# Optimization experiments

Measured on AMD Instinct MI355X. Metric: run time of the kernel, lower is better.

Reference implementation:

```python
import jax, jax.numpy as jnp
from jax import lax
import numpy as np

B, T, N = 32, 64, 128
D = 64            # d_model = d_in
C = 2 * D + 1     # combined dim = 129
CK = C // 8       # per-head q/k dim = 16
H = 2             # num_heads
QD = 5            # query_vector_dim
NE = 8            # node_emb_dim
PLM = 768         # plm_rep_dim
ALPHA = 0.5       # rarity_alpha
NEG = -9e15       # masked_fill value from source


def setup_inputs() -> dict:
    key = jax.random.key(0)
    ks = jax.random.split(key, 20)

    def u(i, shape, fan):
        s = float(np.sqrt(1.0 / fan))
        return jax.random.uniform(ks[i], shape, jnp.float32, -s, s)

    return dict(
        obs_emb=jax.random.normal(ks[0], (B, T, N, D), jnp.float32),
        observed_mask=(jax.random.uniform(ks[1], (B, T, N)) < 0.3).astype(jnp.float32),
        avg_interval=jax.random.uniform(ks[2], (B, T, N), jnp.float32, 0.0, 10.0),
        var_plm_rep_tensor=jax.random.normal(ks[3], (N, PLM), jnp.float32),
        lengths=jax.random.randint(ks[4], (B, 1), T // 2, T + 1).astype(jnp.int32),
        rarity_W=jax.random.normal(ks[5], (N, N), jnp.float32),
        pf_W1=u(6, (PLM, 2 * D), PLM), pf_b1=jnp.zeros((2 * D,), jnp.float32),
        pf_W2=u(7, (2 * D, QD), 2 * D), pf_b2=jnp.zeros((QD,), jnp.float32),
        pg_W1=u(8, (PLM, 2 * D), PLM), pg_b1=jnp.zeros((2 * D,), jnp.float32),
        pg_W2=u(9, (2 * D, NE), 2 * D), pg_b2=jnp.zeros((NE,), jnp.float32),
        rst_W=u(10, (QD, C, D), C), rst_b=u(11, (QD, D), QD),
        upd_W=u(12, (QD, C, D), C), upd_b=u(13, (QD, D), QD),
        cand_W=u(14, (QD, C, D), C), cand_b=u(15, (QD, D), QD),
        q_W=u(16, (H, C, CK), C), q_b=jnp.zeros((H, CK), jnp.float32),
        k_W=u(17, (H, C, CK), C), k_b=jnp.zeros((H, CK), jnp.float32),
        v_W=u(18, (H, C, C), C), v_b=jnp.zeros((H, C), jnp.float32),
    )


def reference(obs_emb, observed_mask, avg_interval, var_plm_rep_tensor,
              rarity_W, pf_W1, pf_b1, pf_W2, pf_b2, pg_W1, pg_b1, pg_W2, pg_b2,
              rst_W, rst_b, upd_W, upd_b, cand_W, cand_b,
              q_W, q_b, k_W, k_b, v_W, v_b, lengths):
    # variable query vectors & node embeddings (identical for every batch element)
    qv = jax.nn.relu(var_plm_rep_tensor @ pf_W1 + pf_b1) @ pf_W2 + pf_b2   # [N,QD]
    ne = jax.nn.relu(var_plm_rep_tensor @ pg_W1 + pg_b1) @ pg_W2 + pg_b2   # [N,NE]
    ne = ne / jnp.maximum(jnp.linalg.norm(ne, axis=-1, keepdims=True), 1e-12)
    adj = jax.nn.softmax(ne @ ne.T, axis=-1)                               # [N,N] static base adjacency
    var_total_obs = observed_mask.sum(axis=1)                               # [B,N]
    I = jnp.eye(N, dtype=obs_emb.dtype)
    inv_sqrt = 1.0 / np.sqrt(CK)

    def gate(z, W, b):
        # hypernetwork-generated per-node affine (MLP_Param): z [B,N,C] -> [B,N,D]
        return jnp.einsum('bnc,qco,nq->bno', z, W, qv) + qv @ b

    def step(carry, xs):
        h, out = carry
        cur_obs, cur_mask, cur_avg, t = xs
        rar = ALPHA * jnp.tanh(cur_avg / (var_total_obs + 1.0))             # [B,N]
        rmat = -rarity_W[None] * jnp.abs(rar[:, :, None] - rar[:, None, :])  # [B,N,N]
        amask = cur_mask[:, :, None] * cur_mask[:, None, :]                  # obs outer-product mask
        cur_adj = adj[None] * (1.0 + rmat) * amask * (1.0 - I) + I
        x = jnp.concatenate([cur_obs, rar[..., None]], axis=-1)             # [B,N,D+1]
        comb = jnp.concatenate([x, h], axis=-1)                              # [B,N,C]
        q = jnp.einsum('bnc,hck->bhnk', comb, q_W) + q_b[None, :, None, :]
        k = jnp.einsum('bnc,hck->bhnk', comb, k_W) + k_b[None, :, None, :]
        v = jnp.einsum('bnc,hcd->bhnd', comb, v_W) + v_b[None, :, None, :]
        s = jnp.einsum('bhnk,bhmk->bhnm', q, k) * inv_sqrt
        s = jax.nn.leaky_relu(s, 0.2)
        s = jnp.where(cur_adj[:, None, :, :] == 0, NEG, s)                   # use_adj_mask=True
        att = jnp.einsum('bhnm,bhmd->bhnd', jax.nn.softmax(s, axis=-1), v).mean(axis=1)  # [B,N,C]
        obs = (cur_mask > 0)[..., None]
        r = jax.nn.sigmoid(gate(att, rst_W, rst_b))
        u = jax.nn.sigmoid(gate(att, upd_W, upd_b))
        h1 = jnp.where(obs, r * h, h)                                        # h[nodes_ind] = r*h[nodes_ind]
        cand = jnp.tanh(gate(jnp.concatenate([x, h1], axis=-1), cand_W, cand_b))
        h2 = jnp.where(obs, (1.0 - u) * h1 + u * cand, h1)                   # scatter update of observed nodes
        fin = (t == lengths[:, 0] - 1)[:, None, None]
        out = jnp.where(fin, h2, out)                                        # capture h at end of each sample
        return (h2, out), None

    h0 = jnp.zeros((B, N, D), obs_emb.dtype)
    xs = (jnp.swapaxes(obs_emb, 0, 1), jnp.swapaxes(observed_mask, 0, 1),
          jnp.swapaxes(avg_interval, 0, 1), jnp.arange(T))
    (_, out), _ = lax.scan(step, (h0, h0), xs)
    return out
```

## Files before the change

### kernel.cpp

```cpp
#include <hip/hip_runtime.h>
#include <math.h>

#define B_   32
#define T_   64
#define N_   128
#define D_   64
#define C_   129
#define CK_  16
#define H_   2
#define QD_  5
#define PLM_ 768

typedef _Float16 h2v __attribute__((ext_vector_type(2)));
typedef _Float16 h4v __attribute__((ext_vector_type(4)));
typedef _Float16 h8  __attribute__((ext_vector_type(8)));
typedef float    f4  __attribute__((ext_vector_type(4)));

constexpr int OFF_QV   = 0;
constexpr int OFF_BE   = 640;
constexpr int OFF_WB2  = OFF_BE + 3*128*64;
constexpr int OFF_VWB2 = OFF_WB2 + 3*128*65*64;
constexpr int OFF_QKB2 = OFF_VWB2 + 2*65*132;
constexpr int OFF_ATTB = OFF_QKB2 + 4*65*16;
constexpr int OFF_VTO  = OFF_ATTB + 132;
constexpr int OFF_H    = OFF_VTO + B_*N_;
constexpr int OFF_CNT  = OFF_H + 2*B_*N_*64;
constexpr int OFF_VWB3 = OFF_CNT + 32;
constexpr int OFF_QKB4 = OFF_VWB3 + 9*9*64*8/2;
constexpr int OFF_QKE  = OFF_QKB4 + 2*2*4*64*8/2;

#if __has_builtin(__builtin_amdgcn_fdot2)
__device__ __forceinline__ float fdot2(h2v a, h2v b, float c) {
    return __builtin_amdgcn_fdot2(a, b, c, false);
}
#else
__device__ __forceinline__ float fdot2(h2v a, h2v b, float c) {
    return c + (float)a.x*(float)b.x + (float)a.y*(float)b.y;
}
#endif


__global__ void k_qv(const float* __restrict__ plm, const float* __restrict__ W1,
                     const float* __restrict__ b1, const float* __restrict__ W2,
                     const float* __restrict__ b2, float* __restrict__ ws) {
    int n = blockIdx.x, j = threadIdx.x;
    __shared__ float hid[128];
    float acc = b1[j];
    for (int p = 0; p < PLM_; ++p) acc += plm[n*PLM_ + p] * W1[p*128 + j];
    hid[j] = fmaxf(acc, 0.f);
    __syncthreads();
    if (j < QD_) {
        float a = b2[j];
        for (int q = 0; q < 128; ++q) a += hid[q] * W2[q*QD_ + j];
        ws[OFF_QV + n*QD_ + j] = a;
    }
}

__global__ void k_weff(const float* __restrict__ rW, const float* __restrict__ uW,
                       const float* __restrict__ cW, const float* __restrict__ rb,
                       const float* __restrict__ ub, const float* __restrict__ cb,
                       float* __restrict__ ws) {
    int g = blockIdx.x >> 7, n = blockIdx.x & 127;
    const float* W  = (g == 0) ? rW : (g == 1) ? uW : cW;
    const float* bb = (g == 0) ? rb : (g == 1) ? ub : cb;
    float qn[QD_];
#pragma unroll
    for (int q = 0; q < QD_; ++q) qn[q] = ws[OFF_QV + n*QD_ + q];
    h2v* WB = (h2v*)(ws + OFF_WB2);
    for (int idx = threadIdx.x; idx < 65*64; idx += 256) {
        int c2 = idx >> 6, o = idx & 63;
        float w0 = 0.f, w1 = 0.f;
#pragma unroll
        for (int q = 0; q < QD_; ++q) w0 += qn[q] * W[(q*C_ + 2*c2)*D_ + o];
        if (2*c2 + 1 < C_) {
#pragma unroll
            for (int q = 0; q < QD_; ++q) w1 += qn[q] * W[(q*C_ + 2*c2 + 1)*D_ + o];
        }
        WB[((g*128 + n)*65 + c2)*64 + o] = h2v{(_Float16)w0, (_Float16)w1};
    }
    if (threadIdx.x < D_) {
        int o = threadIdx.x;
        float acc = 0.f;
#pragma unroll
        for (int q = 0; q < QD_; ++q) acc += qn[q] * bb[q*D_ + o];
        ws[OFF_BE + (g*128 + n)*D_ + o] = acc;
    }
}

__global__ void k_pack(const float* __restrict__ vW, const float* __restrict__ qW,
                       const float* __restrict__ kW, const float* __restrict__ vb,
                       const float* __restrict__ qb, const float* __restrict__ kb,
                       float* __restrict__ ws) {
    int stride = gridDim.x * blockDim.x;
    int t0 = blockIdx.x * blockDim.x + threadIdx.x;
    _Float16* VB = (_Float16*)(ws + OFF_VWB3);
    for (int idx = t0; idx < 9*9*64*8; idx += stride) {
        int j  = idx & 7;
        int l  = (idx >> 3) & 63;
        int rest = idx >> 9;
        int kt = rest % 9, nt = rest / 9;
        int k = kt*32 + (l >> 4)*8 + j;
        int n = nt*16 + (l & 15);
        float v = 0.f;
        if (n < C_) {
            if (k < 264) {
                int h = k / 132, c = k % 132;
                if (c < C_) v = 0.5f * vW[(h*C_ + c)*C_ + n];
            } else if (k == 264) {
                v = 0.5f * (vb[n] + vb[C_ + n]);
            }
        }
        VB[idx] = (_Float16)v;
    }
    _Float16* QK4 = (_Float16*)(ws + OFF_QKB4);
    for (int idx = t0; idx < 2*2*4*64*8; idx += stride) {
        int j = idx & 7, l = (idx >> 3) & 63, kt = (idx >> 9) & 3;
        int h = (idx >> 11) & 1, qk = (idx >> 12) & 1;
        int c = kt*32 + ((l >> 4) & 3)*8 + j, ck = l & 15;
        const float* src = qk ? qW : kW;
        QK4[idx] = (_Float16)src[(h*C_ + c)*CK_ + ck];
    }
    float* QE = ws + OFF_QKE;
    for (int idx = t0; idx < 128; idx += stride) {
        int ck = idx & 15, kind = (idx >> 4) & 1, h = (idx >> 5) & 1, qk = (idx >> 6) & 1;
        const float* src = qk ? qW : kW;
        const float* sb  = qk ? qb : kb;
        QE[idx] = kind ? sb[h*CK_ + ck] : src[(h*C_ + 128)*CK_ + ck];
    }
}

__global__ void k_vto(const float* __restrict__ mask, float* __restrict__ ws) {
    int idx = blockIdx.x * blockDim.x + threadIdx.x;
    if (idx < B_*N_) {
        int b = idx >> 7, n = idx & 127;
        float acc = 0.f;
        for (int t = 0; t < T_; ++t) acc += mask[(b*T_ + t)*N_ + n];
        ws[OFF_VTO + idx] = acc;
    }
}

__global__ void __launch_bounds__(1024, 4) k_main(
    const float* __restrict__ obs, const float* __restrict__ mask,
    const float* __restrict__ avg, const int* __restrict__ lengths,
    const float* __restrict__ qb, const float* __restrict__ kb,
    float* __restrict__ ws, float* __restrict__ out) {
    const int tid = threadIdx.x;
    const int b  = blockIdx.x >> 3;
    const int ng = blockIdx.x & 7;
    const int n0 = ng * 16;

    __shared__ __align__(16) _Float16 comball[128*144];
    __shared__ __align__(16) char regA[8704];
    __shared__ __align__(16) char regB[13824];
    __shared__ float maskL[128];
    __shared__ float h_own[16*64];

    _Float16* sPH    = (_Float16*)regA;
    _Float16* attF   = (_Float16*)regA;
    float*    h1L    = (float*)(regA + 4352);
    _Float16* kall   = (_Float16*)regB;
    _Float16* qf     = (_Float16*)(regB + 12288);
    _Float16* z_lds  = (_Float16*)regB;
    h2v*      candin = (h2v*)regB;

    float* Hx = ws + OFF_H;
    unsigned* CNT = (unsigned*)(ws + OFF_CNT);
    const h2v* WB  = (const h2v*)(ws + OFF_WB2);
    const h8*  VB3 = (const h8*)(ws + OFF_VWB3);
    const h8*  QK4 = (const h8*)(ws + OFF_QKB4);

    for (int i = tid; i < 16*64; i += 1024) h_own[i] = 0.f;
    for (int i = tid; i < 128*15; i += 1024)
        comball[(i/15)*144 + 129 + (i%15)] = (_Float16)0.f;
    const int lenb = lengths[b];
    __syncthreads();

    for (int t = 0; t < T_; ++t) {
        if (t > 0) {
            if (tid == 0) {
                unsigned target = 8u * (unsigned)t;
                while (__hip_atomic_load(&CNT[b], __ATOMIC_RELAXED,
                                         __HIP_MEMORY_SCOPE_AGENT) < target)
                    __builtin_amdgcn_s_sleep(2);
            }
            __syncthreads();
            const float* Hr = Hx + (size_t)((t & 1)*B_ + b)*N_*64;
#pragma unroll
            for (int p = 0; p < 8; ++p) {
                int idx = tid + p*1024;
                int j = idx >> 6, d = idx & 63;
                float hv = ((j >> 4) == ng) ? h_own[(j & 15)*64 + d]
                         : __hip_atomic_load((float*)Hr + idx, __ATOMIC_RELAXED,
                                             __HIP_MEMORY_SCOPE_AGENT);
                comball[j*144 + 65 + d] = (_Float16)hv;
            }
        } else {
#pragma unroll
            for (int p = 0; p < 8; ++p) {
                int idx = tid + p*1024;
                comball[(idx >> 6)*144 + 65 + (idx & 63)] = (_Float16)0.f;
            }
        }
        {
            const float* obsR = obs + (size_t)(b*T_ + t)*N_*D_;
#pragma unroll
            for (int p = 0; p < 8; ++p) {
                int idx = tid + p*1024;
                comball[(idx >> 6)*144 + (idx & 63)] = (_Float16)obsR[idx];
            }
            if (tid < 128) {
                maskL[tid] = mask[(b*T_ + t)*N_ + tid];
                float a = avg[(b*T_ + t)*N_ + tid];
                comball[tid*144 + 64] =
                    (_Float16)(0.5f * tanhf(a / (ws[OFF_VTO + b*N_ + tid] + 1.f)));
            }
        }
        __syncthreads();
        {
            int w = tid >> 6, l = tid & 63, lr = l & 15, lg = l >> 4;
            int nj = (w < 2) ? 2 : 1;
            for (int jb = 0; jb < nj; ++jb) {
                int qk = jb;
                int hh = jb ? w : (w >> 3);
                int rbase = jb ? n0 : (w & 7)*16;
                const h8* Wf = QK4 + ((qk*2 + hh)*4)*64 + l;
                const _Float16* Ab = comball + (rbase + lr)*144;
                f4 acc = {0.f, 0.f, 0.f, 0.f};
#pragma unroll
                for (int kt = 0; kt < 4; ++kt) {
                    h8 a = *(const h8*)(Ab + kt*32 + lg*8);
                    h8 bf = Wf[kt*64];
                    acc = __builtin_amdgcn_mfma_f32_16x16x32_f16(a, bf, acc, 0, 0, 0);
                }
                const float* QE = ws + OFF_QKE + (qk*2 + hh)*32;
                float w128 = QE[lr], wbias = QE[16 + lr];
#pragma unroll
                for (int r = 0; r < 4; ++r) {
                    int row = rbase + lg*4 + r;
                    float v = acc[r] + (float)comball[row*144 + 128] * w128 + wbias;
                    if (jb == 0) kall[(hh*128 + row)*24 + lr] = (_Float16)v;
                    else         qf[(hh*16 + lg*4 + r)*24 + lr] = (_Float16)v;
                }
            }
        }
        __syncthreads();
        {
            int w = tid >> 6, l = tid & 63, lr = l & 15, lg = l >> 4;
            int h = w >> 3, nt = w & 7;
            h8 a = {}, bq = {};
            if (lg < 2) {
                a  = *(const h8*)(qf + (h*16 + lr)*24 + lg*8);
                bq = *(const h8*)(kall + (h*128 + nt*16 + lr)*24 + lg*8);
            }
            f4 s4 = {0.f, 0.f, 0.f, 0.f};
            s4 = __builtin_amdgcn_mfma_f32_16x16x32_f16(a, bq, s4, 0, 0, 0);
            int j = nt*16 + lr;
            float mj = maskL[j];
#pragma unroll
            for (int r = 0; r < 4; ++r) {
                int i = lg*4 + r, ig = n0 + i;
                float v = s4[r] * 0.25f;
                v = v > 0.f ? v : 0.2f*v;
                if (ig != j && (maskL[ig] == 0.f || mj == 0.f)) v = -60000.f;
                sPH[(h*16 + i)*136 + j] = (_Float16)v;
            }
        }
        __syncthreads();
        {
            int wave = tid >> 6, lane = tid & 63;
#pragma unroll
            for (int r = 0; r < 2; ++r) {
                int u = wave*2 + r;
                float x0 = (float)sPH[u*136 + lane], x1 = (float)sPH[u*136 + lane + 64];
                float m = fmaxf(x0, x1);
                for (int off = 32; off > 0; off >>= 1) m = fmaxf(m, __shfl_xor(m, off, 64));
                float e0 = __expf(x0 - m), e1 = __expf(x1 - m);
                float s = e0 + e1;
                for (int off = 32; off > 0; off >>= 1) s += __shfl_xor(s, off, 64);
                float inv = 1.f / s;
                sPH[u*136 + lane] = (_Float16)(e0*inv);
                sPH[u*136 + lane + 64] = (_Float16)(e1*inv);
            }
        }
        __syncthreads();
        {
            if (tid < 384) {
                int i = tid / 24, cc = tid % 24;
                z_lds[i*296 + 264 + cc] = (cc == 0) ? (_Float16)1.0f : (_Float16)0.0f;
            }
            int wv = tid >> 6, l = tid & 63, lr = l & 15, lg = l >> 4;
            for (int tile = wv; tile < 18; tile += 16) {
                int m = tile / 9, n = tile % 9;
                f4 acc = {0.f, 0.f, 0.f, 0.f};
                const _Float16* Arow = sPH + (m*16 + lr)*136 + lg*8;
                const _Float16* Bcol = comball + (lg*8)*144 + n*16 + lr;
#pragma unroll
                for (int kt = 0; kt < 4; ++kt) {
                    h8 a = *(const h8*)(Arow + kt*32);
                    h8 bf;
#pragma unroll
                    for (int j = 0; j < 8; ++j) bf[j] = Bcol[(kt*32 + j)*144];
                    acc = __builtin_amdgcn_mfma_f32_16x16x32_f16(a, bf, acc, 0, 0, 0);
                }
                int cz = n*16 + lr;
                if (cz < 132) {
#pragma unroll
                    for (int r = 0; r < 4; ++r)
                        z_lds[(lg*4 + r)*296 + m*132 + cz] = (_Float16)acc[r];
                }
            }
        }
        __syncthreads();
        {
            int wv = tid >> 6, l = tid & 63, lr = l & 15, lg = l >> 4;
            if (wv < 9) {
                const h8* VB = VB3 + (size_t)wv*9*64 + l;
                f4 acc = {0.f, 0.f, 0.f, 0.f};
                const _Float16* Az = z_lds + lr*296 + lg*8;
#pragma unroll
                for (int kt = 0; kt < 9; ++kt) {
                    h8 a = *(const h8*)(Az + kt*32);
                    h8 bf = VB[kt*64];
                    acc = __builtin_amdgcn_mfma_f32_16x16x32_f16(a, bf, acc, 0, 0, 0);
                }
                int cp = wv*16 + lr;
                if (cp < 132) {
#pragma unroll
                    for (int r = 0; r < 4; ++r)
                        attF[(lg*4 + r)*136 + cp] = (_Float16)acc[r];
                }
            }
        }
        __syncthreads();
        int il = tid >> 6, o = tid & 63, n = n0 + il;
        float uu, h1;
        bool ob;
        {
            const h2v* WR = WB + ((0*128 + n)*65)*64 + o;
            const h2v* WU = WB + ((1*128 + n)*65)*64 + o;
            float aR = ws[OFF_BE + (0*128 + n)*64 + o];
            float aU = ws[OFF_BE + (1*128 + n)*64 + o];
            const h2v* ar = (const h2v*)(attF + il*136);
#pragma unroll 5
            for (int c2 = 0; c2 < 65; ++c2) {
                h2v a2 = ar[c2];
                aR = fdot2(a2, WR[(size_t)c2*64], aR);
                aU = fdot2(a2, WU[(size_t)c2*64], aU);
            }
            float rg = 1.f/(1.f + __expf(-aR));
            uu = 1.f/(1.f + __expf(-aU));
            ob = maskL[n] > 0.f;
            float h0 = h_own[il*64 + o];
            h1 = ob ? rg*h0 : h0;
            h1L[il*66 + o] = h1;
        }
        __syncthreads();
        {
#pragma unroll
            for (int p = 0; p < 2; ++p) {
                int idx = tid + p*1024;
                if (idx < 1040) {
                    int il2 = idx / 65, cw = idx % 65;
                    int c0 = 2*cw, c1 = 2*cw + 1;
                    int j = n0 + il2;
                    float v0 = (c0 < 65) ? (float)comball[j*144 + c0]
                                         : h1L[il2*66 + c0 - 65];
                    float v1 = (c1 < 65) ? (float)comball[j*144 + c1]
                             : ((c1 <= 128) ? h1L[il2*66 + c1 - 65] : 0.f);
                    candin[il2*66 + cw] = h2v{(_Float16)v0, (_Float16)v1};
                }
            }
        }
        __syncthreads();
        {
            const h2v* WC = WB + ((2*128 + n)*65)*64 + o;
            float aC = ws[OFF_BE + (2*128 + n)*64 + o];
            const h2v* zr = candin + il*66;
#pragma unroll 5
            for (int c2 = 0; c2 < 65; ++c2)
                aC = fdot2(zr[c2], WC[(size_t)c2*64], aC);
            float cand = tanhf(aC);
            float h2 = ob ? (1.f - uu)*h1 + uu*cand : h1;
            h_own[il*64 + o] = h2;
            if (t == lenb - 1) out[(size_t)(b*N_ + n)*64 + o] = h2;
            if (t < T_ - 1) {
                float* Hw = Hx + (size_t)(((t + 1) & 1)*B_ + b)*N_*64 + (n0 + il)*64 + o;
                __hip_atomic_store(Hw, h2, __ATOMIC_RELAXED, __HIP_MEMORY_SCOPE_AGENT);
            }
        }
        __syncthreads();
        if (t < T_ - 1 && tid == 0)
            __hip_atomic_fetch_add(&CNT[b], 1u, __ATOMIC_RELAXED, __HIP_MEMORY_SCOPE_AGENT);
    }
}

extern "C" void kernel_launch(void* const* d_in, const int* in_sizes, int n_in,
                              void* d_out, int out_size, void* d_ws, size_t ws_size,
                              hipStream_t stream) {
    (void)in_sizes; (void)n_in; (void)out_size; (void)ws_size;
    const float* obs   = (const float*)d_in[0];
    const float* mask  = (const float*)d_in[1];
    const float* avg   = (const float*)d_in[2];
    const float* plm   = (const float*)d_in[3];
    const int*   lens  = (const int*)d_in[4];
    const float* pfW1  = (const float*)d_in[6];
    const float* pfb1  = (const float*)d_in[7];
    const float* pfW2  = (const float*)d_in[8];
    const float* pfb2  = (const float*)d_in[9];
    const float* rstW  = (const float*)d_in[14];
    const float* rstb  = (const float*)d_in[15];
    const float* updW  = (const float*)d_in[16];
    const float* updb  = (const float*)d_in[17];
    const float* candW = (const float*)d_in[18];
    const float* candb = (const float*)d_in[19];
    const float* qW    = (const float*)d_in[20];
    const float* qb    = (const float*)d_in[21];
    const float* kW    = (const float*)d_in[22];
    const float* kb    = (const float*)d_in[23];
    const float* vW    = (const float*)d_in[24];
    const float* vb    = (const float*)d_in[25];
    float* ws  = (float*)d_ws;
    float* out = (float*)d_out;

    hipMemsetAsync((char*)d_ws + (size_t)OFF_CNT*4, 0, 32*sizeof(unsigned), stream);
    hipLaunchKernelGGL(k_qv,   dim3(128), dim3(128), 0, stream, plm, pfW1, pfb1, pfW2, pfb2, ws);
    hipLaunchKernelGGL(k_weff, dim3(384), dim3(256), 0, stream, rstW, updW, candW, rstb, updb, candb, ws);
    hipLaunchKernelGGL(k_pack, dim3(64),  dim3(256), 0, stream, vW, qW, kW, vb, qb, kb, ws);
    hipLaunchKernelGGL(k_vto,  dim3(16),  dim3(256), 0, stream, mask, ws);

    void* args[] = {(void*)&obs, (void*)&mask, (void*)&avg, (void*)&lens,
                    (void*)&qb, (void*)&kb, (void*)&ws, (void*)&out};
    hipLaunchCooperativeKernel((void*)k_main, dim3(256), dim3(1024), args, 0, stream);
}
```

Baseline: 1.759 ms.

## Compute GRU gates with MFMA over shared weights scaled by query vector

Replaces the per-node effective gate weights (qv-contracted, packed fp16 dot2 loops per node) with shared raw gate weights packed in MFMA fragment layout. The activation rows are scaled by each node's query-vector component inside the K loop, so the reset/update and candidate gates become 16x16x32 MFMA tiles instead of scalar fdot2 loops. It also prefetches the next timestep's obs/mask/avg into registers after the barrier and keeps the mask in a spare comball column. This trades much smaller weight traffic and scalar ALU work for extra barriers, fp16 scaling of activations, and larger LDS padding.

After: 2.761 ms. 1.57x slower.

```diff
diff --git a/kernel.cpp b/kernel.cpp
--- a/kernel.cpp
+++ b/kernel.cpp
@@ -12,13 +12,14 @@
 #define PLM_ 768
 
 typedef _Float16 h2v __attribute__((ext_vector_type(2)));
-typedef _Float16 h4v __attribute__((ext_vector_type(4)));
 typedef _Float16 h8  __attribute__((ext_vector_type(8)));
 typedef float    f4  __attribute__((ext_vector_type(4)));
 
 constexpr int OFF_QV   = 0;
 constexpr int OFF_BE   = 640;
 constexpr int OFF_WB2  = OFF_BE + 3*128*64;
+constexpr int OFF_GRU  = OFF_WB2;
+constexpr int OFF_GC   = OFF_GRU + 8*25*64*8/2;
 constexpr int OFF_VWB2 = OFF_WB2 + 3*128*65*64;
 constexpr int OFF_QKB2 = OFF_VWB2 + 2*65*132;
 constexpr int OFF_ATTB = OFF_QKB2 + 4*65*16;
@@ -28,16 +29,6 @@
 constexpr int OFF_VWB3 = OFF_CNT + 32;
 constexpr int OFF_QKB4 = OFF_VWB3 + 9*9*64*8/2;
 constexpr int OFF_QKE  = OFF_QKB4 + 2*2*4*64*8/2;
-
-#if __has_builtin(__builtin_amdgcn_fdot2)
-__device__ __forceinline__ float fdot2(h2v a, h2v b, float c) {
-    return __builtin_amdgcn_fdot2(a, b, c, false);
-}
-#else
-__device__ __forceinline__ float fdot2(h2v a, h2v b, float c) {
-    return c + (float)a.x*(float)b.x + (float)a.y*(float)b.y;
-}
-#endif
 
 
 __global__ void k_qv(const float* __restrict__ plm, const float* __restrict__ W1,
@@ -56,34 +47,39 @@
     }
 }
 
-__global__ void k_weff(const float* __restrict__ rW, const float* __restrict__ uW,
+__global__ void k_gate(const float* __restrict__ rW, const float* __restrict__ uW,
                        const float* __restrict__ cW, const float* __restrict__ rb,
                        const float* __restrict__ ub, const float* __restrict__ cb,
                        float* __restrict__ ws) {
-    int g = blockIdx.x >> 7, n = blockIdx.x & 127;
-    const float* W  = (g == 0) ? rW : (g == 1) ? uW : cW;
-    const float* bb = (g == 0) ? rb : (g == 1) ? ub : cb;
-    float qn[QD_];
-#pragma unroll
-    for (int q = 0; q < QD_; ++q) qn[q] = ws[OFF_QV + n*QD_ + q];
-    h2v* WB = (h2v*)(ws + OFF_WB2);
-    for (int idx = threadIdx.x; idx < 65*64; idx += 256) {
-        int c2 = idx >> 6, o = idx & 63;
-        float w0 = 0.f, w1 = 0.f;
-#pragma unroll
-        for (int q = 0; q < QD_; ++q) w0 += qn[q] * W[(q*C_ + 2*c2)*D_ + o];
-        if (2*c2 + 1 < C_) {
-#pragma unroll
-            for (int q = 0; q < QD_; ++q) w1 += qn[q] * W[(q*C_ + 2*c2 + 1)*D_ + o];
-        }
-        WB[((g*128 + n)*65 + c2)*64 + o] = h2v{(_Float16)w0, (_Float16)w1};
-    }
-    if (threadIdx.x < D_) {
-        int o = threadIdx.x;
+    int stride = gridDim.x * blockDim.x;
+    int t0 = blockIdx.x * blockDim.x + threadIdx.x;
+    _Float16* GRU = (_Float16*)(ws + OFF_GRU);
+    for (int idx = t0; idx < 8*25*512; idx += stride) {
+        int j = idx & 7, l = (idx >> 3) & 63;
+        int fk = idx >> 9, kt = fk % 25, ot = fk / 25;
+        int k = kt*32 + ((l >> 4) & 3)*8 + j;
+        int q = k / 160, c = k % 160;
+        int oc = ot*16 + (l & 15);
+        const float* W = (oc < 64) ? rW : uW;
+        int o = oc & 63;
+        GRU[idx] = (_Float16)((c < C_) ? W[(q*C_ + c)*D_ + o] : 0.f);
+    }
+    _Float16* GC = (_Float16*)(ws + OFF_GC);
+    for (int idx = t0; idx < 4*25*512; idx += stride) {
+        int j = idx & 7, l = (idx >> 3) & 63;
+        int fk = idx >> 9, kt = fk % 25, ot = fk / 25;
+        int k = kt*32 + ((l >> 4) & 3)*8 + j;
+        int q = k / 160, c = k % 160;
+        int o = ot*16 + (l & 15);
+        GC[idx] = (_Float16)((c < C_) ? cW[(q*C_ + c)*D_ + o] : 0.f);
+    }
+    for (int idx = t0; idx < 3*128*64; idx += stride) {
+        int o = idx & 63, n = (idx >> 6) & 127, g = idx >> 13;
+        const float* bb = (g == 0) ? rb : (g == 1) ? ub : cb;
         float acc = 0.f;
 #pragma unroll
-        for (int q = 0; q < QD_; ++q) acc += qn[q] * bb[q*D_ + o];
-        ws[OFF_BE + (g*128 + n)*D_ + o] = acc;
+        for (int q = 0; q < QD_; ++q) acc += ws[OFF_QV + n*QD_ + q] * bb[q*D_ + o];
+        ws[OFF_BE + idx] = acc;
     }
 }
 
@@ -149,30 +145,50 @@
     const int ng = blockIdx.x & 7;
     const int n0 = ng * 16;
 
-    __shared__ __align__(16) _Float16 comball[128*144];
+    __shared__ __align__(16) _Float16 comball[128*152];
     __shared__ __align__(16) char regA[8704];
-    __shared__ __align__(16) char regB[13824];
-    __shared__ float maskL[128];
+    __shared__ __align__(16) char regB[13312];
     __shared__ float h_own[16*64];
 
     _Float16* sPH    = (_Float16*)regA;
     _Float16* attF   = (_Float16*)regA;
-    float*    h1L    = (float*)(regA + 4352);
+    _Float16* candin = (_Float16*)regA;
     _Float16* kall   = (_Float16*)regB;
     _Float16* qf     = (_Float16*)(regB + 12288);
     _Float16* z_lds  = (_Float16*)regB;
-    h2v*      candin = (h2v*)regB;
+    float*    aRUs   = (float*)regB;
+    float*    candS  = (float*)regB;
 
     float* Hx = ws + OFF_H;
     unsigned* CNT = (unsigned*)(ws + OFF_CNT);
-    const h2v* WB  = (const h2v*)(ws + OFF_WB2);
-    const h8*  VB3 = (const h8*)(ws + OFF_VWB3);
-    const h8*  QK4 = (const h8*)(ws + OFF_QKB4);
+    const h8* VB3 = (const h8*)(ws + OFF_VWB3);
+    const h8* QK4 = (const h8*)(ws + OFF_QKB4);
+    const h8* GRUf = (const h8*)(ws + OFF_GRU);
+    const h8* GCf  = (const h8*)(ws + OFF_GC);
 
     for (int i = tid; i < 16*64; i += 1024) h_own[i] = 0.f;
-    for (int i = tid; i < 128*15; i += 1024)
-        comball[(i/15)*144 + 129 + (i%15)] = (_Float16)0.f;
+    for (int i = tid; i < 128*23; i += 1024)
+        comball[(i/23)*152 + 129 + (i%23)] = (_Float16)0.f;
     const int lenb = lengths[b];
+
+    _Float16 qvh[5];
+    {
+        int lr0 = tid & 15;
+#pragma unroll
+        for (int q = 0; q < QD_; ++q)
+            qvh[q] = (_Float16)ws[OFF_QV + (n0 + lr0)*QD_ + q];
+    }
+    float pf[8], pfm = 0.f, pfa = 0.f, vtoinv = 0.f;
+    {
+        const float* obsR = obs + (size_t)(b*T_)*N_*D_;
+#pragma unroll
+        for (int p = 0; p < 8; ++p) pf[p] = obsR[tid + p*1024];
+        if (tid < 128) {
+            pfm = mask[(size_t)(b*T_)*N_ + tid];
+            pfa = avg[(size_t)(b*T_)*N_ + tid];
+            vtoinv = 1.f / (ws[OFF_VTO + b*N_ + tid] + 1.f);
+        }
+    }
     __syncthreads();
 
     for (int t = 0; t < T_; ++t) {
@@ -192,27 +208,24 @@
                 float hv = ((j >> 4) == ng) ? h_own[(j & 15)*64 + d]
                          : __hip_atomic_load((float*)Hr + idx, __ATOMIC_RELAXED,
                                              __HIP_MEMORY_SCOPE_AGENT);
-                comball[j*144 + 65 + d] = (_Float16)hv;
+                comball[j*152 + 65 + d] = (_Float16)hv;
             }
         } else {
 #pragma unroll
             for (int p = 0; p < 8; ++p) {
                 int idx = tid + p*1024;
-                comball[(idx >> 6)*144 + 65 + (idx & 63)] = (_Float16)0.f;
-            }
-        }
-        {
-            const float* obsR = obs + (size_t)(b*T_ + t)*N_*D_;
+                comball[(idx >> 6)*152 + 65 + (idx & 63)] = (_Float16)0.f;
+            }
+        }
+        {
 #pragma unroll
             for (int p = 0; p < 8; ++p) {
                 int idx = tid + p*1024;
-                comball[(idx >> 6)*144 + (idx & 63)] = (_Float16)obsR[idx];
+                comball[(idx >> 6)*152 + (idx & 63)] = (_Float16)pf[p];
             }
             if (tid < 128) {
-                maskL[tid] = mask[(b*T_ + t)*N_ + tid];
-                float a = avg[(b*T_ + t)*N_ + tid];
-                comball[tid*144 + 64] =
-                    (_Float16)(0.5f * tanhf(a / (ws[OFF_VTO + b*N_ + tid] + 1.f)));
+                comball[tid*152 + 150] = (_Float16)pfm;
+                comball[tid*152 + 64] = (_Float16)(0.5f * tanhf(pfa * vtoinv));
             }
         }
         __syncthreads();
@@ -224,7 +237,7 @@
                 int hh = jb ? w : (w >> 3);
                 int rbase = jb ? n0 : (w & 7)*16;
                 const h8* Wf = QK4 + ((qk*2 + hh)*4)*64 + l;
-                const _Float16* Ab = comball + (rbase + lr)*144;
+                const _Float16* Ab = comball + (rbase + lr)*152;
                 f4 acc = {0.f, 0.f, 0.f, 0.f};
 #pragma unroll
                 for (int kt = 0; kt < 4; ++kt) {
@@ -237,9 +250,9 @@
 #pragma unroll
                 for (int r = 0; r < 4; ++r) {
                     int row = rbase + lg*4 + r;
-                    float v = acc[r] + (float)comball[row*144 + 128] * w128 + wbias;
+                    float v = acc[r] + (float)comball[row*152 + 128] * w128 + wbias;
                     if (jb == 0) kall[(hh*128 + row)*24 + lr] = (_Float16)v;
-                    else         qf[(hh*16 + lg*4 + r)*24 + lr] = (_Float16)v;
+                    else         qf[(hh*16 + lg*4 + r)*16 + lr] = (_Float16)v;
                 }
             }
         }
@@ -249,19 +262,20 @@
             int h = w >> 3, nt = w & 7;
             h8 a = {}, bq = {};
             if (lg < 2) {
-                a  = *(const h8*)(qf + (h*16 + lr)*24 + lg*8);
+                a  = *(const h8*)(qf + (h*16 + lr)*16 + lg*8);
                 bq = *(const h8*)(kall + (h*128 + nt*16 + lr)*24 + lg*8);
             }
             f4 s4 = {0.f, 0.f, 0.f, 0.f};
             s4 = __builtin_amdgcn_mfma_f32_16x16x32_f16(a, bq, s4, 0, 0, 0);
             int j = nt*16 + lr;
-            float mj = maskL[j];
+            float mj = (float)comball[j*152 + 150];
 #pragma unroll
             for (int r = 0; r < 4; ++r) {
                 int i = lg*4 + r, ig = n0 + i;
                 float v = s4[r] * 0.25f;
                 v = v > 0.f ? v : 0.2f*v;
-                if (ig != j && (maskL[ig] == 0.f || mj == 0.f)) v = -60000.f;
+                if (ig != j && ((float)comball[ig*152 + 150] == 0.f || mj == 0.f))
+                    v = -60000.f;
                 sPH[(h*16 + i)*136 + j] = (_Float16)v;
             }
         }
@@ -293,13 +307,13 @@
                 int m = tile / 9, n = tile % 9;
                 f4 acc = {0.f, 0.f, 0.f, 0.f};
                 const _Float16* Arow = sPH + (m*16 + lr)*136 + lg*8;
-                const _Float16* Bcol = comball + (lg*8)*144 + n*16 + lr;
+                const _Float16* Bcol = comball + (lg*8)*152 + n*16 + lr;
 #pragma unroll
                 for (int kt = 0; kt < 4; ++kt) {
                     h8 a = *(const h8*)(Arow + kt*32);
                     h8 bf;
 #pragma unroll
-                    for (int j = 0; j < 8; ++j) bf[j] = Bcol[(kt*32 + j)*144];
+                    for (int j = 0; j < 8; ++j) bf[j] = Bcol[(kt*32 + j)*152];
                     acc = __builtin_amdgcn_mfma_f32_16x16x32_f16(a, bf, acc, 0, 0, 0);
                 }
                 int cz = n*16 + lr;
@@ -327,59 +341,76 @@
                 if (cp < 132) {
 #pragma unroll
                     for (int r = 0; r < 4; ++r)
-                        attF[(lg*4 + r)*136 + cp] = (_Float16)acc[r];
-                }
+                        attF[(lg*4 + r)*168 + cp] = (_Float16)acc[r];
+                }
+            } else {
+                int idx = (wv - 9)*64 + l;
+                attF[(idx & 15)*168 + 132 + (idx >> 4)] = (_Float16)0.f;
+            }
+        }
+        __syncthreads();
+        {
+            int w = tid >> 6, l = tid & 63, lr = l & 15, lg = l >> 4;
+            if (w < 8) {
+                const h8* BF = GRUf + (size_t)w*25*64 + l;
+                const _Float16* Ab = attF + lr*168;
+                f4 acc = {0.f, 0.f, 0.f, 0.f};
+#pragma unroll
+                for (int kt = 0; kt < 25; ++kt) {
+                    h8 av = *(const h8*)(Ab + (kt % 5)*32 + lg*8);
+                    _Float16 s = qvh[kt / 5];
+                    h8 am;
+#pragma unroll
+                    for (int j = 0; j < 8; ++j) am[j] = av[j] * s;
+                    acc = __builtin_amdgcn_mfma_f32_16x16x32_f16(am, BF[kt*64], acc, 0, 0, 0);
+                }
+#pragma unroll
+                for (int r = 0; r < 4; ++r)
+                    aRUs[(lg*4 + r)*128 + w*16 + lr] = acc[r];
             }
         }
         __syncthreads();
         int il = tid >> 6, o = tid & 63, n = n0 + il;
-        float uu, h1;
+        float uu, h1, be2;
         bool ob;
         {
-            const h2v* WR = WB + ((0*128 + n)*65)*64 + o;
-            const h2v* WU = WB + ((1*128 + n)*65)*64 + o;
-            float aR = ws[OFF_BE + (0*128 + n)*64 + o];
-            float aU = ws[OFF_BE + (1*128 + n)*64 + o];
-            const h2v* ar = (const h2v*)(attF + il*136);
-#pragma unroll 5
-            for (int c2 = 0; c2 < 65; ++c2) {
-                h2v a2 = ar[c2];
-                aR = fdot2(a2, WR[(size_t)c2*64], aR);
-                aU = fdot2(a2, WU[(size_t)c2*64], aU);
-            }
+            float aR = aRUs[il*128 + o]      + ws[OFF_BE + (0*128 + n)*64 + o];
+            float aU = aRUs[il*128 + 64 + o] + ws[OFF_BE + (1*128 + n)*64 + o];
+            be2 = ws[OFF_BE + (2*128 + n)*64 + o];
             float rg = 1.f/(1.f + __expf(-aR));
             uu = 1.f/(1.f + __expf(-aU));
-            ob = maskL[n] > 0.f;
+            ob = (float)comball[n*152 + 150] > 0.f;
             float h0 = h_own[il*64 + o];
             h1 = ob ? rg*h0 : h0;
-            h1L[il*66 + o] = h1;
-        }
-        __syncthreads();
-        {
-#pragma unroll
-            for (int p = 0; p < 2; ++p) {
-                int idx = tid + p*1024;
-                if (idx < 1040) {
-                    int il2 = idx / 65, cw = idx % 65;
-                    int c0 = 2*cw, c1 = 2*cw + 1;
-                    int j = n0 + il2;
-                    float v0 = (c0 < 65) ? (float)comball[j*144 + c0]
-                                         : h1L[il2*66 + c0 - 65];
-                    float v1 = (c1 < 65) ? (float)comball[j*144 + c1]
-                             : ((c1 <= 128) ? h1L[il2*66 + c1 - 65] : 0.f);
-                    candin[il2*66 + cw] = h2v{(_Float16)v0, (_Float16)v1};
-                }
-            }
-        }
-        __syncthreads();
-        {
-            const h2v* WC = WB + ((2*128 + n)*65)*64 + o;
-            float aC = ws[OFF_BE + (2*128 + n)*64 + o];
-            const h2v* zr = candin + il*66;
-#pragma unroll 5
-            for (int c2 = 0; c2 < 65; ++c2)
-                aC = fdot2(zr[c2], WC[(size_t)c2*64], aC);
-            float cand = tanhf(aC);
+            candin[il*168 + o] = comball[n*152 + o];
+            if (o == 0) candin[il*168 + 64] = comball[n*152 + 64];
+            candin[il*168 + 65 + o] = (_Float16)h1;
+            if (o >= 1 && o < 32) candin[il*168 + 128 + o] = (_Float16)0.f;
+        }
+        __syncthreads();
+        {
+            int w = tid >> 6, l = tid & 63, lr = l & 15, lg = l >> 4;
+            if (w < 4) {
+                const h8* BF = GCf + (size_t)w*25*64 + l;
+                const _Float16* Ab = candin + lr*168;
+                f4 acc = {0.f, 0.f, 0.f, 0.f};
+#pragma unroll
+                for (int kt = 0; kt < 25; ++kt) {
+                    h8 av = *(const h8*)(Ab + (kt % 5)*32 + lg*8);
+                    _Float16 s = qvh[kt / 5];
+                    h8 am;
+#pragma unroll
+                    for (int j = 0; j < 8; ++j) am[j] = av[j] * s;
+                    acc = __builtin_amdgcn_mfma_f32_16x16x32_f16(am, BF[kt*64], acc, 0, 0, 0);
+                }
+#pragma unroll
+                for (int r = 0; r < 4; ++r)
+                    candS[(lg*4 + r)*64 + w*16 + lr] = acc[r];
+            }
+        }
+        __syncthreads();
+        {
+            float cand = tanhf(candS[il*64 + o] + be2);
             float h2 = ob ? (1.f - uu)*h1 + uu*cand : h1;
             h_own[il*64 + o] = h2;
             if (t == lenb - 1) out[(size_t)(b*N_ + n)*64 + o] = h2;
@@ -391,6 +422,16 @@
         __syncthreads();
         if (t < T_ - 1 && tid == 0)
             __hip_atomic_fetch_add(&CNT[b], 1u, __ATOMIC_RELAXED, __HIP_MEMORY_SCOPE_AGENT);
+        {
+            int tp = (t < T_ - 1) ? t + 1 : t;
+            const float* obsN = obs + (size_t)(b*T_ + tp)*N_*D_;
+#pragma unroll
+            for (int p = 0; p < 8; ++p) pf[p] = obsN[tid + p*1024];
+            if (tid < 128) {
+                pfm = mask[(size_t)(b*T_ + tp)*N_ + tid];
+                pfa = avg[(size_t)(b*T_ + tp)*N_ + tid];
+            }
+        }
     }
 }
 
@@ -424,7 +465,7 @@
 
     hipMemsetAsync((char*)d_ws + (size_t)OFF_CNT*4, 0, 32*sizeof(unsigned), stream);
     hipLaunchKernelGGL(k_qv,   dim3(128), dim3(128), 0, stream, plm, pfW1, pfb1, pfW2, pfb2, ws);
-    hipLaunchKernelGGL(k_weff, dim3(384), dim3(256), 0, stream, rstW, updW, candW, rstb, updb, candb, ws);
+    hipLaunchKernelGGL(k_gate, dim3(256), dim3(256), 0, stream, rstW, updW, candW, rstb, updb, candb, ws);
     hipLaunchKernelGGL(k_pack, dim3(64),  dim3(256), 0, stream, vW, qW, kW, vb, qb, kb, ws);
     hipLaunchKernelGGL(k_vto,  dim3(16),  dim3(256), 0, stream, mask, ws);
 
```

## Pack gate weights as h8 vectors and prefetch next-step inputs into registers

Applied to the files above, without the earlier changes.

Gate weights are repacked from h2v pairs into 16 chunks of 8 fp16 values per output, with the 129th column stored separately in fp32. The gate dot products then use 128-bit loads and a 4x fdot2 chain instead of 65 scalar h2v loads. The candidate input buffer moves to regA with a 136-element row stride so it can be read as h8. The next timestep's obs, mask and avg values are prefetched into registers at the end of each step so their global-load latency overlaps the inter-block wait, and the VTO reciprocal is hoisted out of the loop. The prefetch costs extra registers per thread in a kernel launched with 1024 threads.

Result: slower. 4.470 ms (+154.1%).

```diff
diff --git a/kernel.cpp b/kernel.cpp
--- a/kernel.cpp
+++ b/kernel.cpp
@@ -12,13 +12,13 @@
 #define PLM_ 768
 
 typedef _Float16 h2v __attribute__((ext_vector_type(2)));
-typedef _Float16 h4v __attribute__((ext_vector_type(4)));
 typedef _Float16 h8  __attribute__((ext_vector_type(8)));
 typedef float    f4  __attribute__((ext_vector_type(4)));
 
 constexpr int OFF_QV   = 0;
 constexpr int OFF_BE   = 640;
 constexpr int OFF_WB2  = OFF_BE + 3*128*64;
+constexpr int OFF_WT   = OFF_WB2 + 3*128*16*64*4;
 constexpr int OFF_VWB2 = OFF_WB2 + 3*128*65*64;
 constexpr int OFF_QKB2 = OFF_VWB2 + 2*65*132;
 constexpr int OFF_ATTB = OFF_QKB2 + 4*65*16;
@@ -38,6 +38,14 @@
     return c + (float)a.x*(float)b.x + (float)a.y*(float)b.y;
 }
 #endif
+
+__device__ __forceinline__ float fdot8(h8 a, h8 w, float c) {
+    c = fdot2(h2v{a[0], a[1]}, h2v{w[0], w[1]}, c);
+    c = fdot2(h2v{a[2], a[3]}, h2v{w[2], w[3]}, c);
+    c = fdot2(h2v{a[4], a[5]}, h2v{w[4], w[5]}, c);
+    c = fdot2(h2v{a[6], a[7]}, h2v{w[6], w[7]}, c);
+    return c;
+}
 
 
 __global__ void k_qv(const float* __restrict__ plm, const float* __restrict__ W1,
@@ -66,24 +74,30 @@
     float qn[QD_];
 #pragma unroll
     for (int q = 0; q < QD_; ++q) qn[q] = ws[OFF_QV + n*QD_ + q];
-    h2v* WB = (h2v*)(ws + OFF_WB2);
-    for (int idx = threadIdx.x; idx < 65*64; idx += 256) {
-        int c2 = idx >> 6, o = idx & 63;
-        float w0 = 0.f, w1 = 0.f;
-#pragma unroll
-        for (int q = 0; q < QD_; ++q) w0 += qn[q] * W[(q*C_ + 2*c2)*D_ + o];
-        if (2*c2 + 1 < C_) {
-#pragma unroll
-            for (int q = 0; q < QD_; ++q) w1 += qn[q] * W[(q*C_ + 2*c2 + 1)*D_ + o];
-        }
-        WB[((g*128 + n)*65 + c2)*64 + o] = h2v{(_Float16)w0, (_Float16)w1};
+    h8* WB = (h8*)(ws + OFF_WB2);
+    for (int idx = threadIdx.x; idx < 16*64; idx += 256) {
+        int cc = idx >> 6, o = idx & 63;
+        h8 w;
+#pragma unroll
+        for (int j = 0; j < 8; ++j) {
+            int c = cc*8 + j;
+            float acc = 0.f;
+#pragma unroll
+            for (int q = 0; q < QD_; ++q) acc += qn[q] * W[(q*C_ + c)*D_ + o];
+            w[j] = (_Float16)acc;
+        }
+        WB[((size_t)(g*128 + n)*16 + cc)*64 + o] = w;
     }
     if (threadIdx.x < D_) {
         int o = threadIdx.x;
-        float acc = 0.f;
-#pragma unroll
-        for (int q = 0; q < QD_; ++q) acc += qn[q] * bb[q*D_ + o];
-        ws[OFF_BE + (g*128 + n)*D_ + o] = acc;
+        float wt = 0.f, acc = 0.f;
+#pragma unroll
+        for (int q = 0; q < QD_; ++q) {
+            wt  += qn[q] * W[(q*C_ + 128)*D_ + o];
+            acc += qn[q] * bb[q*D_ + o];
+        }
+        ws[OFF_WT + (g*128 + n)*64 + o] = wt;
+        ws[OFF_BE + (g*128 + n)*64 + o] = acc;
     }
 }
 
@@ -157,22 +171,34 @@
 
     _Float16* sPH    = (_Float16*)regA;
     _Float16* attF   = (_Float16*)regA;
+    _Float16* candin = (_Float16*)regA;
     float*    h1L    = (float*)(regA + 4352);
     _Float16* kall   = (_Float16*)regB;
     _Float16* qf     = (_Float16*)(regB + 12288);
     _Float16* z_lds  = (_Float16*)regB;
-    h2v*      candin = (h2v*)regB;
 
     float* Hx = ws + OFF_H;
     unsigned* CNT = (unsigned*)(ws + OFF_CNT);
-    const h2v* WB  = (const h2v*)(ws + OFF_WB2);
-    const h8*  VB3 = (const h8*)(ws + OFF_VWB3);
-    const h8*  QK4 = (const h8*)(ws + OFF_QKB4);
+    const h8* WB8 = (const h8*)(ws + OFF_WB2);
+    const h8* VB3 = (const h8*)(ws + OFF_VWB3);
+    const h8* QK4 = (const h8*)(ws + OFF_QKB4);
 
     for (int i = tid; i < 16*64; i += 1024) h_own[i] = 0.f;
     for (int i = tid; i < 128*15; i += 1024)
         comball[(i/15)*144 + 129 + (i%15)] = (_Float16)0.f;
     const int lenb = lengths[b];
+
+    float pf[8], pfm = 0.f, pfa = 0.f, vtoinv = 0.f;
+    {
+        const float* obsR = obs + (size_t)(b*T_)*N_*D_;
+#pragma unroll
+        for (int p = 0; p < 8; ++p) pf[p] = obsR[tid + p*1024];
+        if (tid < 128) {
+            pfm = mask[(size_t)(b*T_)*N_ + tid];
+            pfa = avg[(size_t)(b*T_)*N_ + tid];
+            vtoinv = 1.f / (ws[OFF_VTO + b*N_ + tid] + 1.f);
+        }
+    }
     __syncthreads();
 
     for (int t = 0; t < T_; ++t) {
@@ -202,17 +228,14 @@
             }
         }
         {
-            const float* obsR = obs + (size_t)(b*T_ + t)*N_*D_;
 #pragma unroll
             for (int p = 0; p < 8; ++p) {
                 int idx = tid + p*1024;
-                comball[(idx >> 6)*144 + (idx & 63)] = (_Float16)obsR[idx];
+                comball[(idx >> 6)*144 + (idx & 63)] = (_Float16)pf[p];
             }
             if (tid < 128) {
-                maskL[tid] = mask[(b*T_ + t)*N_ + tid];
-                float a = avg[(b*T_ + t)*N_ + tid];
-                comball[tid*144 + 64] =
-                    (_Float16)(0.5f * tanhf(a / (ws[OFF_VTO + b*N_ + tid] + 1.f)));
+                maskL[tid] = pfm;
+                comball[tid*144 + 64] = (_Float16)(0.5f * tanhf(pfa * vtoinv));
             }
         }
         __syncthreads();
@@ -336,17 +359,20 @@
         float uu, h1;
         bool ob;
         {
-            const h2v* WR = WB + ((0*128 + n)*65)*64 + o;
-            const h2v* WU = WB + ((1*128 + n)*65)*64 + o;
+            const h8* WR = WB8 + ((size_t)(0*128 + n)*16)*64 + o;
+            const h8* WU = WB8 + ((size_t)(1*128 + n)*16)*64 + o;
             float aR = ws[OFF_BE + (0*128 + n)*64 + o];
             float aU = ws[OFF_BE + (1*128 + n)*64 + o];
-            const h2v* ar = (const h2v*)(attF + il*136);
-#pragma unroll 5
-            for (int c2 = 0; c2 < 65; ++c2) {
-                h2v a2 = ar[c2];
-                aR = fdot2(a2, WR[(size_t)c2*64], aR);
-                aU = fdot2(a2, WU[(size_t)c2*64], aU);
-            }
+            const h8* ar = (const h8*)(attF + il*136);
+#pragma unroll
+            for (int cc = 0; cc < 16; ++cc) {
+                h8 a8 = ar[cc];
+                aR = fdot8(a8, WR[(size_t)cc*64], aR);
+                aU = fdot8(a8, WU[(size_t)cc*64], aU);
+            }
+            float a128 = (float)attF[il*136 + 128];
+            aR += a128 * ws[OFF_WT + (0*128 + n)*64 + o];
+            aU += a128 * ws[OFF_WT + (1*128 + n)*64 + o];
             float rg = 1.f/(1.f + __expf(-aR));
             uu = 1.f/(1.f + __expf(-aU));
             ob = maskL[n] > 0.f;
@@ -356,6 +382,7 @@
         }
         __syncthreads();
         {
+            h2v* cd = (h2v*)candin;
 #pragma unroll
             for (int p = 0; p < 2; ++p) {
                 int idx = tid + p*1024;
@@ -364,21 +391,22 @@
                     int c0 = 2*cw, c1 = 2*cw + 1;
                     int j = n0 + il2;
                     float v0 = (c0 < 65) ? (float)comball[j*144 + c0]
-                                         : h1L[il2*66 + c0 - 65];
+                             : ((c0 <= 128) ? h1L[il2*66 + c0 - 65] : 0.f);
                     float v1 = (c1 < 65) ? (float)comball[j*144 + c1]
                              : ((c1 <= 128) ? h1L[il2*66 + c1 - 65] : 0.f);
-                    candin[il2*66 + cw] = h2v{(_Float16)v0, (_Float16)v1};
-                }
-            }
-        }
-        __syncthreads();
-        {
-            const h2v* WC = WB + ((2*128 + n)*65)*64 + o;
+                    cd[il2*68 + cw] = h2v{(_Float16)v0, (_Float16)v1};
+                }
+            }
+        }
+        __syncthreads();
+        {
+            const h8* WC = WB8 + ((size_t)(2*128 + n)*16)*64 + o;
             float aC = ws[OFF_BE + (2*128 + n)*64 + o];
-            const h2v* zr = candin + il*66;
-#pragma unroll 5
-            for (int c2 = 0; c2 < 65; ++c2)
-                aC = fdot2(zr[c2], WC[(size_t)c2*64], aC);
+            const h8* zr = (const h8*)(candin + il*136);
+#pragma unroll
+            for (int cc = 0; cc < 16; ++cc)
+                aC = fdot8(zr[cc], WC[(size_t)cc*64], aC);
+            aC += (float)candin[il*136 + 128] * ws[OFF_WT + (2*128 + n)*64 + o];
             float cand = tanhf(aC);
             float h2 = ob ? (1.f - uu)*h1 + uu*cand : h1;
             h_own[il*64 + o] = h2;
@@ -391,6 +419,16 @@
         __syncthreads();
         if (t < T_ - 1 && tid == 0)
             __hip_atomic_fetch_add(&CNT[b], 1u, __ATOMIC_RELAXED, __HIP_MEMORY_SCOPE_AGENT);
+        {
+            int tp = (t < T_ - 1) ? t + 1 : t;
+            const float* obsN = obs + (size_t)(b*T_ + tp)*N_*D_;
+#pragma unroll
+            for (int p = 0; p < 8; ++p) pf[p] = obsN[tid + p*1024];
+            if (tid < 128) {
+                pfm = mask[(size_t)(b*T_ + tp)*N_ + tid];
+                pfa = avg[(size_t)(b*T_ + tp)*N_ + tid];
+            }
+        }
     }
 }
 
```
